# Kernel tuning notes

Hardware: AMD Instinct MI355X
Metric: run time of the kernel (lower is better)

## Reference

```python
import jax, jax.numpy as jnp
import numpy as np
from jax import lax

B, TX, RX, RATE, DIMZ, HID, DIRS = 8192, 32, 32, 2, 64, 128, 2
S, FEAT = 2 * TX, 2 * TX + 1
BN_EPS = 1e-5
GD_STEP = 1e-6   # hardcoded in original forward
GD_ITERS = 10    # hardcoded in original forward


def setup_inputs() -> dict:
    key = jax.random.key(0)
    ks = jax.random.split(key, 9)
    sc = 1.0 / np.sqrt(HID)
    return {
        "y": jax.random.normal(ks[0], (B, 2 * RX), jnp.float32),
        "H": jax.random.normal(ks[1], (B, 2 * RX, 2 * TX), jnp.float32),
        "x_raw": jax.random.randint(ks[2], (B, 2 * TX, 1), 0, 2 ** RATE).astype(jnp.float32),
        "gru_w_ih": jax.random.uniform(ks[3], (DIRS, 3 * HID, FEAT), jnp.float32, -sc, sc),
        "gru_w_hh": jax.random.uniform(ks[4], (DIRS, 3 * HID, HID), jnp.float32, -sc, sc),
        "gru_b_ih": jax.random.uniform(ks[5], (DIRS, 3 * HID), jnp.float32, -sc, sc),
        "gru_b_hh": jax.random.uniform(ks[6], (DIRS, 3 * HID), jnp.float32, -sc, sc),
        "w_Wz": jax.random.normal(ks[7], (DIMZ, DIRS * HID), jnp.float32),
        "w_Wx": jax.random.normal(ks[8], (DIMZ, DIRS * HID), jnp.float32),
        "bn_gamma": jnp.ones((2 * TX,), jnp.float32),
        "bn_beta": jnp.zeros((2 * TX,), jnp.float32),
        "step_size": 1,
        "iterations": 10,
    }


def _gru_dir(x_seq, wih, whh, bih, bhh):
    # x_seq: (S, B, F); PyTorch GRU cell equations
    xg = jnp.einsum('sbf,gf->sbg', x_seq, wih) + bih  # (S, B, 3H)

    def step(h, xg_t):
        hg = h @ whh.T + bhh
        xr, xz, xn = jnp.split(xg_t, 3, axis=-1)
        hr, hz, hn = jnp.split(hg, 3, axis=-1)
        r = jax.nn.sigmoid(xr + hr)
        z = jax.nn.sigmoid(xz + hz)
        n = jnp.tanh(xn + r * hn)
        h = (1.0 - z) * n + z * h
        return h, h

    h0 = jnp.zeros((x_seq.shape[1], whh.shape[1]), x_seq.dtype)
    _, out = lax.scan(step, h0, xg)
    return out  # (S, B, H)


def reference(y, H, x_raw, gru_w_ih, gru_w_hh, gru_b_ih, gru_b_hh,
              w_Wz, w_Wx, bn_gamma, bn_beta, step_size, iterations):
    # Hty: (B, 2tx, 1), HtH: (B, 2tx, 2tx)
    Hty = jnp.einsum('brt,br->bt', H, y)[..., None]
    HtH = jnp.einsum('brt,bru->btu', H, H)

    # BatchNorm1d over channel dim 2tx (stats over batch and last dim)
    feats = jnp.concatenate([HtH, Hty], axis=-1)  # (B, 2tx, 2tx+1)
    mu = feats.mean(axis=(0, 2), keepdims=True)
    var = feats.var(axis=(0, 2), keepdims=True)
    feats = (feats - mu) / jnp.sqrt(var + BN_EPS)
    feats = feats * bn_gamma[None, :, None] + bn_beta[None, :, None]

    # bidirectional GRU over seq dim (seq_len = 2tx)
    x_seq = jnp.transpose(feats, (1, 0, 2))  # (S, B, F)
    fwd = _gru_dir(x_seq, gru_w_ih[0], gru_w_hh[0], gru_b_ih[0], gru_b_hh[0])
    bwd = _gru_dir(x_seq[::-1], gru_w_ih[1], gru_w_hh[1], gru_b_ih[1], gru_b_hh[1])[::-1]
    go = jnp.concatenate([fwd, bwd], axis=-1)  # (S, B, 2H)

    w_z = jnp.transpose(go @ w_Wz.T, (1, 2, 0))  # (B, dim_z, S)
    w_x = jnp.transpose(go @ w_Wx.T, (1, 0, 2))  # (B, S, dim_z)

    x_hat0 = 2.0 * x_raw - (2.0 ** RATE) + 1.0  # QAM symbols
    z0 = w_z @ x_hat0  # (B, dim_z, 1)

    # gradient-descent loop (step_size/iterations args ignored, as in source)
    wxt = jnp.swapaxes(w_x, 1, 2)        # (B, dim_z, 2tx)
    wxt_hty = wxt @ Hty                  # (B, dim_z, 1)
    whhw = wxt @ (HtH @ w_x)             # (B, dim_z, dim_z)
    two_step = 2.0 * GD_STEP

    def gd(zh, _):
        return zh + two_step * (wxt_hty - whhw @ zh), None

    z_hat, _ = lax.scan(gd, z0, None, length=GD_ITERS)
    return w_x @ z_hat  # (B, 2tx, 1)
```

## Files before the change

kernel.cpp:

```cpp
#include <hip/hip_runtime.h>
#include <math.h>


typedef __attribute__((ext_vector_type(8))) short s8v;
typedef __attribute__((ext_vector_type(4))) float f4v;

__device__ __forceinline__ short f2bf(float x) {
  unsigned u = __float_as_uint(x);
  u += 0x7fffu + ((u >> 16) & 1u);
  return (short)(u >> 16);
}
__device__ __forceinline__ float bf2f(short h) {
  return __uint_as_float(((unsigned)(unsigned short)h) << 16);
}
__device__ __forceinline__ void fma4(float4& c, float a, const float4 w) {
  c.x += a*w.x; c.y += a*w.y; c.z += a*w.z; c.w += a*w.w;
}
__device__ __forceinline__ float vget(const float4& v, int i) { return ((const float*)&v)[i]; }

__device__ __forceinline__ void gload16(const void* g, void* l) {
  __builtin_amdgcn_global_load_lds(
      (const __attribute__((address_space(1))) void*)g,
      (__attribute__((address_space(3))) void*)l, 16, 0, 0);
}

#define MFMA(A, B, C) __builtin_amdgcn_mfma_f32_16x16x32_bf16((A), (B), (C), 0, 0, 0)

__global__ __launch_bounds__(256) void k_feats(
    const float* __restrict__ Hm, const float* __restrict__ y,
    short* __restrict__ fragX, float* __restrict__ htyU, float* __restrict__ bnacc)
{
  __shared__ __align__(16) float Hl[64][68];
  __shared__ float yl[64];
  __shared__ float s1[64], s2[64];
  const int b = blockIdx.x;
  const int tid = threadIdx.x;
  const float* Hb = Hm + (size_t)b*4096;
  for (int i = tid; i < 4096; i += 256) Hl[i>>6][i&63] = Hb[i];
  if (tid < 64) { yl[tid] = y[b*64+tid]; s1[tid] = 0.f; s2[tid] = 0.f; }
  __syncthreads();

  if (tid < 64) {
    float acc = 0.f;
    for (int r = 0; r < 64; ++r) acc += Hl[r][tid]*yl[r];
    htyU[tid*8192 + b] = acc;
    atomicAdd(&s1[tid], acc);
    atomicAdd(&s2[tid], acc*acc);
  }
  const int tg = tid & 15, ug = tid >> 4;
  float4 acc4[4];
  acc4[0]=acc4[1]=acc4[2]=acc4[3]=make_float4(0.f,0.f,0.f,0.f);
  for (int r = 0; r < 64; ++r) {
    const float4 tv = *(const float4*)&Hl[r][4*tg];
    const float4 uv = *(const float4*)&Hl[r][4*ug];
    #pragma unroll
    for (int tt=0;tt<4;++tt) fma4(acc4[tt], vget(tv,tt), uv);
  }
  const int mt   = (b >> 4) & 3;
  const int brow = b & 15;
  const int u0   = 4*ug;
  short* fbase = fragX + (size_t)(b >> 6)*64*8192
               + (mt*2 + (u0 >> 5))*512 + (brow + 16*((u0 >> 3) & 3))*8 + (u0 & 7);
  #pragma unroll
  for (int tt=0;tt<4;++tt) {
    const int t = 4*tg+tt;
    float sv=0.f, sq=0.f;
    short hib[4], lob[4];
    #pragma unroll
    for (int uu=0;uu<4;++uu) {
      const float v = vget(acc4[tt],uu);
      const short hi = f2bf(v);
      hib[uu] = hi; lob[uu] = f2bf(v - bf2f(hi));
      sv += v; sq += v*v;
    }
    short* dst = fbase + (size_t)t*8192;
    *(short4*)dst          = make_short4(hib[0],hib[1],hib[2],hib[3]);
    *(short4*)(dst + 4096) = make_short4(lob[0],lob[1],lob[2],lob[3]);
    sv += __shfl_down(sv,32); sq += __shfl_down(sq,32);
    sv += __shfl_down(sv,16); sq += __shfl_down(sq,16);
    if ((tid & 63) < 16) { atomicAdd(&s1[t], sv); atomicAdd(&s2[t], sq); }
  }
  __syncthreads();
  if (tid < 64) {
    atomicAdd(&bnacc[tid*16],      s1[tid]);
    atomicAdd(&bnacc[(64+tid)*16], s2[tid]);
  }
}

__global__ void k_bnfin(const float* __restrict__ bnacc, const float* __restrict__ gam,
                        const float* __restrict__ bet, float* __restrict__ bnac)
{
  const int t = threadIdx.x;
  if (t < 64) {
    const float inv = 1.f/532480.f;
    const float mu  = bnacc[t*16]*inv;
    const float var = bnacc[(64+t)*16]*inv - mu*mu;
    const float a = gam[t]*rsqrtf(var + 1e-5f);
    bnac[t] = a;
    bnac[64+t] = bet[t] - mu*a;
  }
}

__global__ __launch_bounds__(256) void k_prep(
    const float* __restrict__ wih, const float* __restrict__ whh,
    const float* __restrict__ Wz, const float* __restrict__ Wx,
    short* __restrict__ Wg, short* __restrict__ W2g, float* __restrict__ rowsum)
{
  const int i = blockIdx.x*256 + threadIdx.x;
  if (i < 294912) {
    const int dd = i / 147456, r = i % 147456;
    const int sp = r / 73728, r2 = r % 73728;
    const int chunk = r2 / 512, e = r2 % 512;
    const int lane = e >> 3, ii = e & 7;
    const int nt = chunk / 6, kt = chunk % 6;
    const int n = nt*16 + (lane & 15);
    const int k = kt*32 + (lane >> 4)*8 + ii;
    const float v = (k < 64) ? wih[dd*24960 + n*65 + k]
                             : whh[dd*49152 + n*128 + (k - 64)];
    const short hi = f2bf(v);
    Wg[i] = sp ? f2bf(v - bf2f(hi)) : hi;
  } else if (i < 360448) {
    const int t = i - 294912;
    const int dd = t / 32768, r = t % 32768;
    const int sp = r / 16384, r2 = r % 16384;
    const int chunk = r2 / 512, e = r2 % 512;
    const int lane = e >> 3, ii = e & 7;
    const int nt2 = chunk / 4, kt = chunk % 4;
    const int n2 = nt2*16 + (lane & 15);
    const int k = kt*32 + (lane >> 4)*8 + ii;
    const float v = (n2 < 64) ? Wx[n2*256 + dd*128 + k]
                              : Wz[(n2 - 64)*256 + dd*128 + k];
    const short hi = f2bf(v);
    W2g[t] = sp ? f2bf(v - bf2f(hi)) : hi;
  } else if (i < 361216) {
    const int t = i - 360448;
    const int dd = t / 384, g = t % 384;
    float ssum = 0.f;
    for (int f = 0; f < 65; ++f) ssum += wih[dd*24960 + g*65 + f];
    rowsum[t] = ssum;
  }
}

__global__ __launch_bounds__(512, 2) void k_scan(
    const short* __restrict__ fragX, const float* __restrict__ htyU,
    const float* __restrict__ xraw,
    const short* __restrict__ Wg, const short* __restrict__ W2g,
    const float* __restrict__ bih, const float* __restrict__ bhh,
    const float* __restrict__ rowsum, const float* __restrict__ bnac,
    const float* __restrict__ wih,
    float* __restrict__ wx_out, float* __restrict__ z0_out)
{
  __shared__ __align__(16) short Axb[8192];
  __shared__ __align__(16) short Ahb[16384];
  __shared__ __align__(16) float xl[64][36];
  __shared__ __align__(16) float gcl[1536];
  __shared__ __align__(16) float z0l[32][68];
  __shared__ float bna[128];

  const int tid = threadIdx.x;
  const int l   = tid & 63;
  const int w   = __builtin_amdgcn_readfirstlane(tid >> 6);
  const int tile = blockIdx.x >> 1, d = blockIdx.x & 1;
  const int b0  = tile * 32;
  const int T64 = tile >> 1, hh = tile & 1;
  const int l15 = l & 15, lq = l >> 4;
  const int j   = 16*w + l15;
  const int zcol = 16*(w & 3) + l15;

  const short* Wgd = Wg  + d*147456;
  const short* W2d = W2g + d*32768;
  float* wxo = wx_out + (size_t)d * (8192ull*4096ull);
  float* z0o = z0_out + (size_t)d * (8192ull*64ull);

  s8v BR[6][2], BZ[6][2], BN[6][2], BP[4][2];
  #pragma unroll
  for (int kt = 0; kt < 6; ++kt)
    #pragma unroll
    for (int sp = 0; sp < 2; ++sp) {
      BR[kt][sp] = *(const s8v*)&Wgd[((sp*24 + w     )*6 + kt)*512 + l*8];
      BZ[kt][sp] = *(const s8v*)&Wgd[((sp*24 + 8 + w )*6 + kt)*512 + l*8];
      BN[kt][sp] = *(const s8v*)&Wgd[((sp*24 + 16 + w)*6 + kt)*512 + l*8];
    }
  #pragma unroll
  for (int kt = 0; kt < 4; ++kt)
    #pragma unroll
    for (int sp = 0; sp < 2; ++sp)
      BP[kt][sp] = *(const s8v*)&W2d[((sp*8 + w)*4 + kt)*512 + l*8];

  const int hw_base = (j >> 5)*512 + ((j >> 3) & 3)*128 + (j & 7);

  const int c_sp  = w >> 2, c_mtl = (w >> 1) & 1, c_kt = w & 1;
  const size_t choff = (size_t)c_sp*8192 + (size_t)(2*(2*hh + c_mtl) + c_kt)*1024;
  const char* fragT = (const char*)fragX + (size_t)T64*1048576ull;

  for (int i = tid; i < 16384; i += 512) Ahb[i] = 0;
  for (int i = tid; i < 2048; i += 512) {
    const int bl = i >> 6, s = i & 63;
    xl[s][bl] = 2.f*xraw[(size_t)(b0 + bl)*64 + s] - 3.f;
  }
  if (tid < 128) {
    const int jj = tid;
    float* g = &gcl[jj*12];
    g[0] = rowsum[d*384 + jj];
    g[1] = rowsum[d*384 + 128 + jj];
    g[2] = rowsum[d*384 + 256 + jj];
    g[3] = bih[d*384 + jj]       + bhh[d*384 + jj];
    g[4] = bih[d*384 + 128 + jj] + bhh[d*384 + 128 + jj];
    g[5] = bih[d*384 + 256 + jj];
    g[6] = bhh[d*384 + 256 + jj];
    g[7] = wih[d*24960 + jj*65 + 64];
    g[8] = wih[d*24960 + (128 + jj)*65 + 64];
    g[9] = wih[d*24960 + (256 + jj)*65 + 64];
    g[10] = 0.f; g[11] = 0.f;
  }
  for (int i = tid; i < 32*68; i += 512) ((float*)z0l)[i] = 0.f;
  if (tid < 128) bna[tid] = bnac[tid];

  f4v hprev[2];
  hprev[0] = (f4v)0.f; hprev[1] = (f4v)0.f;

  {
    const int s0 = d ? 63 : 0;
    gload16(fragT + (size_t)s0*16384 + choff + l*16, (char*)Axb + w*1024);
  }
  __syncthreads();

  for (int it = 0; it < 64; ++it) {
    const int s  = d ? 63 - it : it;
    const int sn = (it < 63) ? (d ? s - 1 : s + 1) : s;

    const short* AxR = Axb + ((it & 1) << 12);
    char*        AxW = (char*)Axb + (((it + 1) & 1) << 13);
    const short* AhR = Ahb + (((it + 1) & 1) << 13);
    short*       AhW = Ahb + ((it & 1) << 13);

    gload16(fragT + (size_t)sn*16384 + choff + l*16, AxW + w*1024);

    const float a_s = bna[s], c_s = bna[64 + s];
    const volatile float* gj = gcl + j*12;
    const float crK  = c_s*gj[0] + gj[3];
    const float czK  = c_s*gj[1] + gj[4];
    const float cnK  = c_s*gj[2] + gj[5];
    const float BHN  = gj[6];
    const float w64r = gj[7], w64z = gj[8], w64n = gj[9];

    #pragma unroll
    for (int mtl = 0; mtl < 2; ++mtl) {
      const float4 av4 = *(const float4*)&htyU[s*8192 + b0 + mtl*16 + lq*4];
      f4v Crx = (f4v)0.f, Czx = (f4v)0.f, Cnx = (f4v)0.f;
      f4v Crh = (f4v)0.f, Czh = (f4v)0.f, Cnh = (f4v)0.f;
      #pragma unroll
      for (int kt = 0; kt < 2; ++kt) {
        const s8v axh = *(const s8v*)&AxR[mtl*1024 + kt*512 + l*8];
        const s8v axl = *(const s8v*)&AxR[2048 + mtl*1024 + kt*512 + l*8];
        Crx = MFMA(axh, BR[kt][0], Crx); Crx = MFMA(axh, BR[kt][1], Crx); Crx = MFMA(axl, BR[kt][0], Crx);
        Czx = MFMA(axh, BZ[kt][0], Czx); Czx = MFMA(axh, BZ[kt][1], Czx); Czx = MFMA(axl, BZ[kt][0], Czx);
        Cnx = MFMA(axh, BN[kt][0], Cnx); Cnx = MFMA(axh, BN[kt][1], Cnx); Cnx = MFMA(axl, BN[kt][0], Cnx);
      }
      #pragma unroll
      for (int kh = 0; kh < 4; ++kh) {
        const s8v ahh = *(const s8v*)&AhR[mtl*2048 + kh*512 + l*8];
        const s8v ahl = *(const s8v*)&AhR[4096 + mtl*2048 + kh*512 + l*8];
        const int kt = 2 + kh;
        Crh = MFMA(ahh, BR[kt][0], Crh); Crh = MFMA(ahh, BR[kt][1], Crh); Crh = MFMA(ahl, BR[kt][0], Crh);
        Czh = MFMA(ahh, BZ[kt][0], Czh); Czh = MFMA(ahh, BZ[kt][1], Czh); Czh = MFMA(ahl, BZ[kt][0], Czh);
        Cnh = MFMA(ahh, BN[kt][0], Cnh); Cnh = MFMA(ahh, BN[kt][1], Cnh); Cnh = MFMA(ahl, BN[kt][0], Cnh);
      }
      f4v av; av[0]=av4.x; av[1]=av4.y; av[2]=av4.z; av[3]=av4.w;
      Crx += av * w64r; Czx += av * w64z; Cnx += av * w64n;
      #pragma unroll
      for (int e = 0; e < 4; ++e) {
        const float rr  = 1.f/(1.f + __expf(-(a_s*Crx[e] + Crh[e] + crK)));
        const float zz  = 1.f/(1.f + __expf(-(a_s*Czx[e] + Czh[e] + czK)));
        const float pre = a_s*Cnx[e] + cnK + rr*(Cnh[e] + BHN);
        const float ax2 = fabsf(pre);
        const float ee  = __expf(-2.f*ax2);
        const float nn  = copysignf((1.f - ee)/(1.f + ee), pre);
        hprev[mtl][e] = (1.f - zz)*nn + zz*hprev[mtl][e];
      }
    }

    #pragma unroll
    for (int mtl = 0; mtl < 2; ++mtl)
      #pragma unroll
      for (int e = 0; e < 4; ++e) {
        const float hv = hprev[mtl][e];
        const short hi = f2bf(hv);
        const int ad = mtl*2048 + hw_base + (lq*4 + e)*8;
        AhW[ad] = hi;
        AhW[4096 + ad] = f2bf(hv - bf2f(hi));
      }
    __syncthreads();

    #pragma unroll
    for (int mtl = 0; mtl < 2; ++mtl) {
      f4v Cp = (f4v)0.f;
      #pragma unroll
      for (int kt = 0; kt < 4; ++kt) {
        const s8v ahh = *(const s8v*)&AhW[mtl*2048 + kt*512 + l*8];
        const s8v ahl = *(const s8v*)&AhW[4096 + mtl*2048 + kt*512 + l*8];
        Cp = MFMA(ahh, BP[kt][0], Cp);
        Cp = MFMA(ahh, BP[kt][1], Cp);
        Cp = MFMA(ahl, BP[kt][0], Cp);
      }
      if (w < 4) {
        #pragma unroll
        for (int e = 0; e < 4; ++e)
          wxo[(size_t)(b0 + mtl*16 + lq*4 + e)*4096 + s*64 + 16*w + l15] = Cp[e];
      } else {
        #pragma unroll
        for (int e = 0; e < 4; ++e) {
          const int bl = mtl*16 + lq*4 + e;
          z0l[bl][zcol] += xl[s][bl] * Cp[e];
        }
      }
    }
  }
  if (w >= 4) {
    #pragma unroll
    for (int mtl = 0; mtl < 2; ++mtl)
      #pragma unroll
      for (int e = 0; e < 4; ++e) {
        const int bl = mtl*16 + lq*4 + e;
        z0o[(size_t)(b0 + bl)*64 + zcol] = z0l[bl][zcol];
      }
  }
}

__global__ __launch_bounds__(256) void k_gd(
    const float* __restrict__ Hm, const float* __restrict__ y,
    const float* __restrict__ wxf, const float* __restrict__ wxb,
    const float* __restrict__ z0f, const float* __restrict__ z0b,
    float* __restrict__ out)
{
  __shared__ __align__(16) float Hl[64][68];
  __shared__ __align__(16) float wx[64][68];
  __shared__ __align__(16) float tmp[64][68];
  __shared__ float yl[64], wh[64], zv[64];
  const int b = blockIdx.x;
  const int tid = threadIdx.x;
  const float* Hb = Hm + (size_t)b*4096;
  for (int i = tid; i < 4096; i += 256) {
    Hl[i>>6][i&63] = Hb[i];
    wx[i>>6][i&63] = wxf[(size_t)b*4096 + i] + wxb[(size_t)b*4096 + i];
  }
  if (tid < 64) {
    yl[tid] = y[b*64+tid];
    zv[tid] = z0f[(size_t)b*64+tid] + z0b[(size_t)b*64+tid];
  }
  __syncthreads();
  const int zq = tid & 15, tq = tid >> 4;
  #pragma unroll
  for (int rr = 0; rr < 4; ++rr) {
    const int r = 4*tq + rr;
    float4 a = make_float4(0.f,0.f,0.f,0.f);
    for (int t = 0; t < 64; ++t) fma4(a, Hl[r][t], *(const float4*)&wx[t][4*zq]);
    *(float4*)&tmp[r][4*zq] = a;
  }
  __syncthreads();
  float (*ww)[68] = Hl;
  #pragma unroll
  for (int ii = 0; ii < 4; ++ii) {
    const int zi = 4*tq + ii;
    float4 a = make_float4(0.f,0.f,0.f,0.f);
    for (int r = 0; r < 64; ++r) fma4(a, tmp[r][zi], *(const float4*)&tmp[r][4*zq]);
    *(float4*)&ww[zi][4*zq] = a;
  }
  if (tid < 64) {
    float acc = 0.f;
    for (int r = 0; r < 64; ++r) acc += tmp[r][tid]*yl[r];
    wh[tid] = acc;
  }
  __syncthreads();
  for (int itr = 0; itr < 10; ++itr) {
    float nz = 0.f;
    if (tid < 64) {
      float mv = 0.f;
      for (int k2 = 0; k2 < 64; ++k2) mv += ww[tid][k2]*zv[k2];
      nz = zv[tid] + 2e-6f*(wh[tid] - mv);
    }
    __syncthreads();
    if (tid < 64) zv[tid] = nz;
    __syncthreads();
  }
  if (tid < 64) {
    float o = 0.f;
    for (int z2 = 0; z2 < 64; ++z2) o += wx[tid][z2]*zv[z2];
    out[(size_t)b*64 + tid] = o;
  }
}

extern "C" void kernel_launch(void* const* d_in, const int* in_sizes, int n_in,
                              void* d_out, int out_size, void* d_ws, size_t ws_size,
                              hipStream_t stream)
{
  const float* y    = (const float*)d_in[0];
  const float* Hm   = (const float*)d_in[1];
  const float* xraw = (const float*)d_in[2];
  const float* wih  = (const float*)d_in[3];
  const float* whh  = (const float*)d_in[4];
  const float* bih  = (const float*)d_in[5];
  const float* bhh  = (const float*)d_in[6];
  const float* Wz   = (const float*)d_in[7];
  const float* Wx   = (const float*)d_in[8];
  const float* gam  = (const float*)d_in[9];
  const float* bet  = (const float*)d_in[10];
  float* out = (float*)d_out;
  float* ws  = (float*)d_ws;

  float* wxf   = ws;
  float* wxb   = wxf + 33554432ull;
  float* z0f   = wxb + 33554432ull;
  float* z0b   = z0f + 524288ull;
  float* htyU  = z0b + 524288ull;
  float* rows  = htyU + 524288ull;
  float* bnacc = rows + 768ull;
  float* bnac  = bnacc + 2048ull;
  short* Wgs   = (short*)(bnac + 128ull);
  short* W2gs  = Wgs + 294912ull;
  short* fragX = W2gs + 65536ull;

  hipMemsetAsync(bnacc, 0, 2048*sizeof(float), stream);
  k_feats <<<8192, 256, 0, stream>>>(Hm, y, fragX, htyU, bnacc);
  k_prep  <<<1412, 256, 0, stream>>>(wih, whh, Wz, Wx, Wgs, W2gs, rows);
  k_bnfin <<<1, 64, 0, stream>>>(bnacc, gam, bet, bnac);
  k_scan  <<<512, 512, 0, stream>>>(fragX, htyU, xraw, Wgs, W2gs,
                                    bih, bhh, rows, bnac, wih, wxf, z0f);
  k_gd    <<<8192, 256, 0, stream>>>(Hm, y, wxf, wxb, z0f, z0b, out);
}
```

Before: 2.175 ms.

## Stream GRU weight fragments from global each step instead of holding in registers

Removes the register-resident weight fragments (BR/BZ/BN/BP, about 160 VGPRs) and reloads them from global/L2 every timestep through an opaque zero offset, which keeps the compiler from hoisting the loads. The loops are reordered so each weight fragment is used for both batch sub-tiles, and launch bounds go from 2 to 4 blocks per CU to raise occupancy. The exchange is much more L1/L2 traffic per timestep and load latency on the serial recurrence critical path. Extra waves may or may not hide that latency.

```diff
diff --git a/kernel.cpp b/kernel.cpp
--- a/kernel.cpp
+++ b/kernel.cpp
@@ -141,7 +141,7 @@
   }
 }
 
-__global__ __launch_bounds__(512, 2) void k_scan(
+__global__ __launch_bounds__(512, 4) void k_scan(
     const short* __restrict__ fragX, const float* __restrict__ htyU,
     const float* __restrict__ xraw,
     const short* __restrict__ Wg, const short* __restrict__ W2g,
@@ -172,20 +172,8 @@
   float* wxo = wx_out + (size_t)d * (8192ull*4096ull);
   float* z0o = z0_out + (size_t)d * (8192ull*64ull);
 
-  s8v BR[6][2], BZ[6][2], BN[6][2], BP[4][2];
-  #pragma unroll
-  for (int kt = 0; kt < 6; ++kt)
-    #pragma unroll
-    for (int sp = 0; sp < 2; ++sp) {
-      BR[kt][sp] = *(const s8v*)&Wgd[((sp*24 + w     )*6 + kt)*512 + l*8];
-      BZ[kt][sp] = *(const s8v*)&Wgd[((sp*24 + 8 + w )*6 + kt)*512 + l*8];
-      BN[kt][sp] = *(const s8v*)&Wgd[((sp*24 + 16 + w)*6 + kt)*512 + l*8];
-    }
-  #pragma unroll
-  for (int kt = 0; kt < 4; ++kt)
-    #pragma unroll
-    for (int sp = 0; sp < 2; ++sp)
-      BP[kt][sp] = *(const s8v*)&W2d[((sp*8 + w)*4 + kt)*512 + l*8];
+  const int wbG = w*3072 + l*8;
+  const int wbP = w*2048 + l*8;
 
   const int hw_base = (j >> 5)*512 + ((j >> 3) & 3)*128 + (j & 7);
 
@@ -229,6 +217,11 @@
     const int s  = d ? 63 - it : it;
     const int sn = (it < 63) ? (d ? s - 1 : s + 1) : s;
 
+    int lz = 0;
+    asm volatile("" : "+v"(lz));
+    const short* Wv  = Wgd + lz;
+    const short* W2v = W2d + lz;
+
     const short* AxR = Axb + ((it & 1) << 12);
     char*        AxW = (char*)Axb + (((it + 1) & 1) << 13);
     const short* AhR = Ahb + (((it + 1) & 1) << 13);
@@ -244,84 +237,109 @@
     const float BHN  = gj[6];
     const float w64r = gj[7], w64z = gj[8], w64n = gj[9];
 
-    #pragma unroll
-    for (int mtl = 0; mtl < 2; ++mtl) {
-      const float4 av4 = *(const float4*)&htyU[s*8192 + b0 + mtl*16 + lq*4];
-      f4v Crx = (f4v)0.f, Czx = (f4v)0.f, Cnx = (f4v)0.f;
-      f4v Crh = (f4v)0.f, Czh = (f4v)0.f, Cnh = (f4v)0.f;
-      #pragma unroll
-      for (int kt = 0; kt < 2; ++kt) {
-        const s8v axh = *(const s8v*)&AxR[mtl*1024 + kt*512 + l*8];
-        const s8v axl = *(const s8v*)&AxR[2048 + mtl*1024 + kt*512 + l*8];
-        Crx = MFMA(axh, BR[kt][0], Crx); Crx = MFMA(axh, BR[kt][1], Crx); Crx = MFMA(axl, BR[kt][0], Crx);
-        Czx = MFMA(axh, BZ[kt][0], Czx); Czx = MFMA(axh, BZ[kt][1], Czx); Czx = MFMA(axl, BZ[kt][0], Czx);
-        Cnx = MFMA(axh, BN[kt][0], Cnx); Cnx = MFMA(axh, BN[kt][1], Cnx); Cnx = MFMA(axl, BN[kt][0], Cnx);
-      }
-      #pragma unroll
-      for (int kh = 0; kh < 4; ++kh) {
-        const s8v ahh = *(const s8v*)&AhR[mtl*2048 + kh*512 + l*8];
-        const s8v ahl = *(const s8v*)&AhR[4096 + mtl*2048 + kh*512 + l*8];
-        const int kt = 2 + kh;
-        Crh = MFMA(ahh, BR[kt][0], Crh); Crh = MFMA(ahh, BR[kt][1], Crh); Crh = MFMA(ahl, BR[kt][0], Crh);
-        Czh = MFMA(ahh, BZ[kt][0], Czh); Czh = MFMA(ahh, BZ[kt][1], Czh); Czh = MFMA(ahl, BZ[kt][0], Czh);
-        Cnh = MFMA(ahh, BN[kt][0], Cnh); Cnh = MFMA(ahh, BN[kt][1], Cnh); Cnh = MFMA(ahl, BN[kt][0], Cnh);
-      }
+    const float4 hty0 = *(const float4*)&htyU[s*8192 + b0 + lq*4];
+    const float4 hty1 = *(const float4*)&htyU[s*8192 + b0 + 16 + lq*4];
+
+    f4v Crx[2], Czx[2], Cnx[2], Crh[2], Czh[2], Cnh[2];
+    #pragma unroll
+    for (int m = 0; m < 2; ++m) {
+      Crx[m]=(f4v)0.f; Czx[m]=(f4v)0.f; Cnx[m]=(f4v)0.f;
+      Crh[m]=(f4v)0.f; Czh[m]=(f4v)0.f; Cnh[m]=(f4v)0.f;
+    }
+    #pragma unroll
+    for (int kt = 0; kt < 6; ++kt) {
+      const s8v bRh = *(const s8v*)&Wv[wbG + kt*512];
+      const s8v bRl = *(const s8v*)&Wv[wbG + 73728 + kt*512];
+      const s8v bZh = *(const s8v*)&Wv[wbG + 24576 + kt*512];
+      const s8v bZl = *(const s8v*)&Wv[wbG + 98304 + kt*512];
+      const s8v bNh = *(const s8v*)&Wv[wbG + 49152 + kt*512];
+      const s8v bNl = *(const s8v*)&Wv[wbG + 122880 + kt*512];
+      if (kt < 2) {
+        #pragma unroll
+        for (int m = 0; m < 2; ++m) {
+          const s8v ah = *(const s8v*)&AxR[m*1024 + kt*512 + l*8];
+          const s8v al = *(const s8v*)&AxR[2048 + m*1024 + kt*512 + l*8];
+          Crx[m]=MFMA(ah,bRh,Crx[m]); Crx[m]=MFMA(ah,bRl,Crx[m]); Crx[m]=MFMA(al,bRh,Crx[m]);
+          Czx[m]=MFMA(ah,bZh,Czx[m]); Czx[m]=MFMA(ah,bZl,Czx[m]); Czx[m]=MFMA(al,bZh,Czx[m]);
+          Cnx[m]=MFMA(ah,bNh,Cnx[m]); Cnx[m]=MFMA(ah,bNl,Cnx[m]); Cnx[m]=MFMA(al,bNh,Cnx[m]);
+        }
+      } else {
+        const int kh = kt - 2;
+        #pragma unroll
+        for (int m = 0; m < 2; ++m) {
+          const s8v ah = *(const s8v*)&AhR[m*2048 + kh*512 + l*8];
+          const s8v al = *(const s8v*)&AhR[4096 + m*2048 + kh*512 + l*8];
+          Crh[m]=MFMA(ah,bRh,Crh[m]); Crh[m]=MFMA(ah,bRl,Crh[m]); Crh[m]=MFMA(al,bRh,Crh[m]);
+          Czh[m]=MFMA(ah,bZh,Czh[m]); Czh[m]=MFMA(ah,bZl,Czh[m]); Czh[m]=MFMA(al,bZh,Czh[m]);
+          Cnh[m]=MFMA(ah,bNh,Cnh[m]); Cnh[m]=MFMA(ah,bNl,Cnh[m]); Cnh[m]=MFMA(al,bNh,Cnh[m]);
+        }
+      }
+    }
+
+    #pragma unroll
+    for (int m = 0; m < 2; ++m) {
+      const float4 av4 = m ? hty1 : hty0;
       f4v av; av[0]=av4.x; av[1]=av4.y; av[2]=av4.z; av[3]=av4.w;
-      Crx += av * w64r; Czx += av * w64z; Cnx += av * w64n;
+      const f4v crx = Crx[m] + av * w64r;
+      const f4v czx = Czx[m] + av * w64z;
+      const f4v cnx = Cnx[m] + av * w64n;
       #pragma unroll
       for (int e = 0; e < 4; ++e) {
-        const float rr  = 1.f/(1.f + __expf(-(a_s*Crx[e] + Crh[e] + crK)));
-        const float zz  = 1.f/(1.f + __expf(-(a_s*Czx[e] + Czh[e] + czK)));
-        const float pre = a_s*Cnx[e] + cnK + rr*(Cnh[e] + BHN);
+        const float rr  = 1.f/(1.f + __expf(-(a_s*crx[e] + Crh[m][e] + crK)));
+        const float zz  = 1.f/(1.f + __expf(-(a_s*czx[e] + Czh[m][e] + czK)));
+        const float pre = a_s*cnx[e] + cnK + rr*(Cnh[m][e] + BHN);
         const float ax2 = fabsf(pre);
         const float ee  = __expf(-2.f*ax2);
         const float nn  = copysignf((1.f - ee)/(1.f + ee), pre);
-        hprev[mtl][e] = (1.f - zz)*nn + zz*hprev[mtl][e];
-      }
-    }
-
-    #pragma unroll
-    for (int mtl = 0; mtl < 2; ++mtl)
+        hprev[m][e] = (1.f - zz)*nn + zz*hprev[m][e];
+      }
+    }
+
+    #pragma unroll
+    for (int m = 0; m < 2; ++m)
       #pragma unroll
       for (int e = 0; e < 4; ++e) {
-        const float hv = hprev[mtl][e];
+        const float hv = hprev[m][e];
         const short hi = f2bf(hv);
-        const int ad = mtl*2048 + hw_base + (lq*4 + e)*8;
+        const int ad = m*2048 + hw_base + (lq*4 + e)*8;
         AhW[ad] = hi;
         AhW[4096 + ad] = f2bf(hv - bf2f(hi));
       }
     __syncthreads();
 
-    #pragma unroll
-    for (int mtl = 0; mtl < 2; ++mtl) {
-      f4v Cp = (f4v)0.f;
+    f4v Cp[2]; Cp[0] = (f4v)0.f; Cp[1] = (f4v)0.f;
+    #pragma unroll
+    for (int kt = 0; kt < 4; ++kt) {
+      const s8v bPh = *(const s8v*)&W2v[wbP + kt*512];
+      const s8v bPl = *(const s8v*)&W2v[wbP + 16384 + kt*512];
       #pragma unroll
-      for (int kt = 0; kt < 4; ++kt) {
-        const s8v ahh = *(const s8v*)&AhW[mtl*2048 + kt*512 + l*8];
-        const s8v ahl = *(const s8v*)&AhW[4096 + mtl*2048 + kt*512 + l*8];
-        Cp = MFMA(ahh, BP[kt][0], Cp);
-        Cp = MFMA(ahh, BP[kt][1], Cp);
-        Cp = MFMA(ahl, BP[kt][0], Cp);
-      }
+      for (int m = 0; m < 2; ++m) {
+        const s8v ah = *(const s8v*)&AhW[m*2048 + kt*512 + l*8];
+        const s8v al = *(const s8v*)&AhW[4096 + m*2048 + kt*512 + l*8];
+        Cp[m]=MFMA(ah,bPh,Cp[m]); Cp[m]=MFMA(ah,bPl,Cp[m]); Cp[m]=MFMA(al,bPh,Cp[m]);
+      }
+    }
+    #pragma unroll
+    for (int m = 0; m < 2; ++m) {
       if (w < 4) {
         #pragma unroll
         for (int e = 0; e < 4; ++e)
-          wxo[(size_t)(b0 + mtl*16 + lq*4 + e)*4096 + s*64 + 16*w + l15] = Cp[e];
+          wxo[(size_t)(b0 + m*16 + lq*4 + e)*4096 + s*64 + 16*w + l15] = Cp[m][e];
       } else {
         #pragma unroll
         for (int e = 0; e < 4; ++e) {
-          const int bl = mtl*16 + lq*4 + e;
-          z0l[bl][zcol] += xl[s][bl] * Cp[e];
+          const int bl = m*16 + lq*4 + e;
+          z0l[bl][zcol] += xl[s][bl] * Cp[m][e];
         }
       }
     }
   }
   if (w >= 4) {
     #pragma unroll
-    for (int mtl = 0; mtl < 2; ++mtl)
+    for (int m = 0; m < 2; ++m)
       #pragma unroll
       for (int e = 0; e < 4; ++e) {
-        const int bl = mtl*16 + lq*4 + e;
+        const int bl = m*16 + lq*4 + e;
         z0o[(size_t)(b0 + bl)*64 + zcol] = z0l[bl][zcol];
       }
   }
```

After: 1.868 ms. 1.16x faster.
